# Kernel optimization log

Hardware: AMD Instinct MI355X
Metric: run time of the kernel (lower is better)

## Reference

```python
import jax, jax.numpy as jnp
import numpy as np

INPUT_SIZE, HIDDEN_SIZE, MEMORY_SIZE, SEQ_LEN, THETA = 512, 1024, 256, 4096, 4096.0
BATCH = 8


def _expm(M):
    # scaling-and-squaring Taylor expm (float64), replaces scipy cont2discrete's expm
    nrm = np.linalg.norm(M, 1)
    s = max(0, int(np.ceil(np.log2(max(nrm, 1.0)))) + 4)
    A = M / (2.0 ** s)
    E = np.eye(M.shape[0])
    T = np.eye(M.shape[0])
    for k in range(1, 24):
        T = T @ A / k
        E = E + T
    for _ in range(s):
        E = E @ E
    return E


def _lmu_H():
    # continuous-time Legendre state-space matrices
    Q = np.arange(MEMORY_SIZE, dtype=np.float64).reshape(-1, 1)
    R = (2.0 * Q + 1.0) / THETA
    i, j = np.meshgrid(Q.ravel(), Q.ravel(), indexing="ij")
    A = R * np.where(i < j, -1.0, (-1.0) ** (i - j + 1))
    B = R * (-1.0) ** Q
    # zero-order-hold discretization with dt=1: expm([[A,B],[0,0]])
    aug = np.zeros((MEMORY_SIZE + 1, MEMORY_SIZE + 1))
    aug[:MEMORY_SIZE, :MEMORY_SIZE] = A
    aug[:MEMORY_SIZE, MEMORY_SIZE:] = B
    Md = _expm(aug)
    Ad = Md[:MEMORY_SIZE, :MEMORY_SIZE].astype(np.float32)
    Bd = Md[:MEMORY_SIZE, MEMORY_SIZE:].astype(np.float32)
    # impulse response: H[:, t] = Ad^t @ Bd  (matches torch impulse() in float32)
    H = np.empty((MEMORY_SIZE, SEQ_LEN), dtype=np.float32)
    h = Bd[:, 0]
    for t in range(SEQ_LEN):
        H[:, t] = h
        h = Ad @ h
    return H


def setup_inputs():
    key = jax.random.key(0)
    k1, k2, k3, k4, k5 = jax.random.split(key, 5)
    x = jax.random.normal(k1, (BATCH, SEQ_LEN, INPUT_SIZE), jnp.float32)
    W_u_w = jax.random.normal(k2, (1, INPUT_SIZE), jnp.float32) / np.float32(np.sqrt(INPUT_SIZE))
    W_u_b = jax.random.normal(k3, (1,), jnp.float32) * 0.01
    W_h_w = jax.random.normal(k4, (HIDDEN_SIZE, MEMORY_SIZE + INPUT_SIZE), jnp.float32) / np.float32(np.sqrt(MEMORY_SIZE + INPUT_SIZE))
    W_h_b = jax.random.normal(k5, (HIDDEN_SIZE,), jnp.float32) * 0.01
    H = jnp.asarray(_lmu_H())
    return {"x": x, "W_u_w": W_u_w, "W_u_b": W_u_b, "W_h_w": W_h_w, "W_h_b": W_h_b, "H": H}


def reference(x, W_u_w, W_u_b, W_h_w, W_h_b, H):
    B, S, D = x.shape
    # u_t = relu(W_u x_t)  -> [B, S, 1]
    u = jax.nn.relu(jnp.einsum("bsd,od->bso", x, W_u_w) + W_u_b)
    # FFT long convolution of u with impulse response H (linear conv via 2S padding)
    fft_u = jnp.fft.rfft(u.transpose(0, 2, 1), n=2 * S, axis=-1)  # [B, 1, S+1]
    fft_H = jnp.fft.rfft(H, n=2 * S, axis=-1)                     # [M, S+1]
    m = jnp.fft.irfft(fft_u * fft_H[None], n=2 * S, axis=-1)[:, :, :S]  # [B, M, S]
    m = m.transpose(0, 2, 1)                                      # [B, S, M]
    # h_t = relu(W_h [m_t; x_t])
    h = jax.nn.relu(jnp.einsum("bsk,hk->bsh", jnp.concatenate([m, x], axis=-1), W_h_w) + W_h_b)
    return h, h[:, -1, :]
```

## Files before the change

kernel.cpp:

```cpp
#include <hip/hip_runtime.h>

typedef _Float16 half8 __attribute__((ext_vector_type(8)));
typedef float f32x4 __attribute__((ext_vector_type(4)));

#define SEQ   4096
#define DIN   512
#define HID   1024
#define KMEM  256
#define NB    8
#define KC    768
#define VP    4352
#define OUT_H_ELEMS 33554432ull

__device__ __forceinline__ void load_lds16(const void* g, void* l) {
  __builtin_amdgcn_global_load_lds(
      (const __attribute__((address_space(1))) unsigned int*)g,
      (__attribute__((address_space(3))) unsigned int*)l, 16, 0, 0);
}

__global__ __launch_bounds__(256) void u_kernel(
    const float* __restrict__ x, const float* __restrict__ Wu,
    const float* __restrict__ Wub,
    const float* __restrict__ Hf, const float* __restrict__ Wf,
    _Float16* __restrict__ xh, _Float16* __restrict__ v2,
    _Float16* __restrict__ Hh, _Float16* __restrict__ Wh)
{
  int tid_g = blockIdx.x * 256 + threadIdx.x;
  if (tid_g < KMEM * SEQ) Hh[tid_g] = (_Float16)Hf[tid_g];
  if (tid_g < HID * KC)   Wh[tid_g] = (_Float16)Wf[tid_g];
  if (tid_g < NB * 8 * 256) {
    int b2 = tid_g >> 11, rem = tid_g & 2047, p = rem >> 8, z = rem & 255;
    int t = (z < p) ? z : 4096 + z;
    v2[((size_t)b2 * 8 + p) * VP + t] = (_Float16)0.f;
  }

  int w = threadIdx.x >> 6, lane = threadIdx.x & 63;
  int row = blockIdx.x * 4 + w;
  const float4* xr = (const float4*)(x + (size_t)row * DIN);
  const float4* wr = (const float4*)Wu;
  float4 a0 = xr[lane * 2], a1 = xr[lane * 2 + 1];
  float4 w0 = wr[lane * 2], w1 = wr[lane * 2 + 1];
  float dot = a0.x * w0.x + a0.y * w0.y + a0.z * w0.z + a0.w * w0.w
            + a1.x * w1.x + a1.y * w1.y + a1.z * w1.z + a1.w * w1.w;
  half8 hv;
  hv[0] = (_Float16)a0.x; hv[1] = (_Float16)a0.y;
  hv[2] = (_Float16)a0.z; hv[3] = (_Float16)a0.w;
  hv[4] = (_Float16)a1.x; hv[5] = (_Float16)a1.y;
  hv[6] = (_Float16)a1.z; hv[7] = (_Float16)a1.w;
  *((half8*)(xh + (size_t)row * DIN + lane * 8)) = hv;
  #pragma unroll
  for (int off = 32; off > 0; off >>= 1) dot += __shfl_xor(dot, off);
  float u = dot + Wub[0];
  u = u > 0.f ? u : 0.f;
  if (lane < 8) {
    int s = row & (SEQ - 1), b = row >> 12;
    v2[(size_t)b * 8 * VP + (size_t)lane * VP + (4095 - s + lane)] = (_Float16)u;
  }
}

__global__ __launch_bounds__(256, 3) void conv_kernel(
    const _Float16* __restrict__ Hh, const _Float16* __restrict__ v2,
    _Float16* __restrict__ mh)
{
  __shared__ _Float16 Bs[2][128 * 64];
  __shared__ _Float16 Aw[2][8 * 208];
  int g = blockIdx.x;
  int cb = g & 15;
  int b = cb >> 1, kt = cb & 1;
  int jj = g >> 4;
  int its = (jj < 16) ? jj : (47 - jj);
  int s0 = its * 128, k0 = kt * 128;
  int tid = threadIdx.x;
  int w = tid >> 6, lane = tid & 63;
  int wr = w >> 1, wc = w & 1;
  int lm = lane & 15, q = lane >> 4;
  const _Float16* v2b = v2 + (size_t)b * 8 * VP;
  int gb = 3968 - s0;

  int aoffs[4];
  #pragma unroll
  for (int mi = 0; mi < 4; mi++) {
    int X = wr * 64 + mi * 16 + lm;
    int p = (X + 1) & 7;
    aoffs[mi] = p * 208 + (127 - X + p) + q * 8;
  }
  int boffs[4];
  #pragma unroll
  for (int ni = 0; ni < 4; ni++) {
    int col = wc * 64 + ni * 16 + lm;
    boffs[ni] = col * 64 + ((q ^ (lm & 7)) << 3);
  }

  int ap = tid / 26, aidx = tid - ap * 26;

  f32x4 acc[4][4] = {};
  int iters = 2 * (its + 1);

  {
    if (tid < 208)
      load_lds16(v2b + (size_t)ap * VP + gb + aidx * 8, Aw[0] + tid * 8);
    #pragma unroll
    for (int p2 = 0; p2 < 4; p2++) {
      int c = p2 * 256 + tid;
      int col = c >> 3, sl = c & 7;
      load_lds16(Hh + (size_t)(k0 + col) * SEQ + ((sl ^ (col & 7)) << 3),
                 Bs[0] + (size_t)c * 8);
    }
  }

  for (int it = 0; it < iters; ++it) {
    int buf = it & 1;
    __syncthreads();
    if (it + 1 < iters) {
      int r0 = (it + 1) * 64;
      if (tid < 208)
        load_lds16(v2b + (size_t)ap * VP + gb + r0 + aidx * 8, Aw[buf ^ 1] + tid * 8);
      #pragma unroll
      for (int p2 = 0; p2 < 4; p2++) {
        int c = p2 * 256 + tid;
        int col = c >> 3, sl = c & 7;
        load_lds16(Hh + (size_t)(k0 + col) * SEQ + r0 + ((sl ^ (col & 7)) << 3),
                   Bs[buf ^ 1] + (size_t)c * 8);
      }
    }
    #pragma unroll
    for (int kq = 0; kq < 2; kq++) {
      half8 af[4], bf[4];
      #pragma unroll
      for (int mi = 0; mi < 4; mi++)
        af[mi] = *((const half8*)(Aw[buf] + aoffs[mi] + kq * 32));
      #pragma unroll
      for (int ni = 0; ni < 4; ni++)
        bf[ni] = *((const half8*)(Bs[buf] + (boffs[ni] ^ (kq << 5))));
      #pragma unroll
      for (int mi = 0; mi < 4; mi++)
        #pragma unroll
        for (int ni = 0; ni < 4; ni++)
          acc[mi][ni] = __builtin_amdgcn_mfma_f32_16x16x32_f16(af[mi], bf[ni], acc[mi][ni], 0, 0, 0);
    }
  }
  size_t rowbase = (size_t)b * SEQ;
  #pragma unroll
  for (int mi = 0; mi < 4; mi++) {
    #pragma unroll
    for (int ni = 0; ni < 4; ni++) {
      int kout = k0 + wc * 64 + ni * 16 + lm;
      #pragma unroll
      for (int r = 0; r < 4; r++) {
        int sout = s0 + wr * 64 + mi * 16 + q * 4 + r;
        mh[(rowbase + sout) * KMEM + kout] = (_Float16)acc[mi][ni][r];
      }
    }
  }
}

__global__ __launch_bounds__(512, 4) void h_kernel(
    const _Float16* __restrict__ mh, const _Float16* __restrict__ xh,
    const _Float16* __restrict__ Wh, const float* __restrict__ Whb,
    float* __restrict__ out)
{
  __shared__ _Float16 As[2][128 * 32];
  __shared__ _Float16 Bs[2][256 * 32];
  int id = blockIdx.x;
  int wgid = (id & 7) * 128 + (id >> 3);
  int mt = wgid >> 2;
  int nt = wgid & 3;
  int tid = threadIdx.x, w = tid >> 6, lane = tid & 63;
  int wr = w >> 2, wc = w & 3;
  int lm = lane & 15, q = lane >> 4;

  int offM, offX;
  {
    int rowA = tid >> 2, chA = tid & 3;
    int swA = chA ^ ((rowA >> 2) & 3);
    offM = (mt * 128 + rowA) * KMEM + swA * 8;
    offX = (mt * 128 + rowA) * DIN  + swA * 8;
  }
  int offB[2];
  #pragma unroll
  for (int r = 0; r < 2; ++r) {
    int c = r * 512 + tid;
    int rowB = c >> 2, chB = c & 3;
    int swB = chB ^ ((rowB >> 2) & 3);
    offB[r] = (nt * 256 + rowB) * KC + swB * 8;
  }

  int qs = (q ^ ((lm >> 2) & 3)) << 3;
  int aoff[4], boff[4];
  #pragma unroll
  for (int mi = 0; mi < 4; ++mi) aoff[mi] = (wr * 64 + mi * 16 + lm) * 32 + qs;
  #pragma unroll
  for (int ni = 0; ni < 4; ++ni) boff[ni] = (wc * 64 + ni * 16 + lm) * 32 + qs;

  f32x4 acc[4][4] = {};
  {
    load_lds16(mh + offM, As[0] + tid * 8);
    #pragma unroll
    for (int r = 0; r < 2; ++r)
      load_lds16(Wh + offB[r], Bs[0] + (size_t)(r * 512 + tid) * 8);
  }

  for (int it = 0; it < 24; ++it) {
    int buf = it & 1;
    __syncthreads();
    if (it + 1 < 24) {
      int kk = (it + 1) * 32;
      const _Float16* srcA = (kk < KMEM) ? (mh + offM + kk)
                                         : (xh + offX + (kk - KMEM));
      load_lds16(srcA, As[buf ^ 1] + tid * 8);
      #pragma unroll
      for (int r = 0; r < 2; ++r)
        load_lds16(Wh + offB[r] + kk, Bs[buf ^ 1] + (size_t)(r * 512 + tid) * 8);
    }
    half8 af[4], bf[4];
    #pragma unroll
    for (int mi = 0; mi < 4; ++mi) af[mi] = *((const half8*)(As[buf] + aoff[mi]));
    #pragma unroll
    for (int ni = 0; ni < 4; ++ni) bf[ni] = *((const half8*)(Bs[buf] + boff[ni]));
    __builtin_amdgcn_s_setprio(1);
    #pragma unroll
    for (int mi = 0; mi < 4; ++mi)
      #pragma unroll
      for (int ni = 0; ni < 4; ++ni)
        acc[mi][ni] = __builtin_amdgcn_mfma_f32_16x16x32_f16(af[mi], bf[ni], acc[mi][ni], 0, 0, 0);
    __builtin_amdgcn_s_setprio(0);
  }

  #pragma unroll
  for (int ni = 0; ni < 4; ni++) {
    int colg = nt * 256 + wc * 64 + ni * 16 + lm;
    float bias = Whb[colg];
    #pragma unroll
    for (int mi = 0; mi < 4; mi++) {
      #pragma unroll
      for (int r = 0; r < 4; r++) {
        int rowg = mt * 128 + wr * 64 + mi * 16 + q * 4 + r;
        float v = acc[mi][ni][r] + bias;
        v = v > 0.f ? v : 0.f;
        __builtin_nontemporal_store(v, &out[(size_t)rowg * HID + colg]);
        if ((rowg & (SEQ - 1)) == SEQ - 1)
          __builtin_nontemporal_store(
              v, &out[OUT_H_ELEMS + (size_t)(rowg >> 12) * HID + colg]);
      }
    }
  }
}

extern "C" void kernel_launch(void* const* d_in, const int* in_sizes, int n_in,
                              void* d_out, int out_size, void* d_ws, size_t ws_size,
                              hipStream_t stream) {
  const float* x   = (const float*)d_in[0];
  const float* Wu  = (const float*)d_in[1];
  const float* Wub = (const float*)d_in[2];
  const float* Whw = (const float*)d_in[3];
  const float* Whb = (const float*)d_in[4];
  const float* Hf  = (const float*)d_in[5];
  float* out = (float*)d_out;

  char* ws = (char*)d_ws;
  _Float16* Hh = (_Float16*)(ws);
  _Float16* Wh = (_Float16*)(ws + 2097152);
  _Float16* v2 = (_Float16*)(ws + 3670016);
  _Float16* xh = (_Float16*)(ws + 4227072);
  _Float16* mh = (_Float16*)(ws + 37781504);

  u_kernel<<<dim3(8192), dim3(256), 0, stream>>>(x, Wu, Wub, Hf, Whw, xh, v2, Hh, Wh);
  conv_kernel<<<dim3(512), dim3(256), 0, stream>>>(Hh, v2, mh);
  h_kernel<<<dim3(1024), dim3(512), 0, stream>>>(mh, xh, Wh, Whb, out);
}
```

Baseline: 305.8 us.

## Load weight fragments directly from global memory and double K-step per stage

The h_kernel GEMM no longer stages the weight (B) tile in LDS. Each wave reads its B fragments straight from global memory into registers. The A tile is staged with a K-step of 64 instead of 32 and a new 8-way XOR swizzle, which halves the loop iterations and barriers. This removes the B-tile LDS traffic and frees LDS for occupancy, but it relies on L1/L2 hits for redundant weight reads across waves and exposes global load latency inside the loop.

```diff
diff --git a/kernel.cpp b/kernel.cpp
--- a/kernel.cpp
+++ b/kernel.cpp
@@ -159,8 +159,8 @@
     const _Float16* __restrict__ Wh, const float* __restrict__ Whb,
     float* __restrict__ out)
 {
-  __shared__ _Float16 As[2][128 * 32];
-  __shared__ _Float16 Bs[2][256 * 32];
+  __shared__ _Float16 As[2][128 * 64];
+
   int id = blockIdx.x;
   int wgid = (id & 7) * 128 + (id >> 3);
   int mt = wgid >> 2;
@@ -169,60 +169,67 @@
   int wr = w >> 2, wc = w & 3;
   int lm = lane & 15, q = lane >> 4;
 
-  int offM, offX;
-  {
-    int rowA = tid >> 2, chA = tid & 3;
-    int swA = chA ^ ((rowA >> 2) & 3);
-    offM = (mt * 128 + rowA) * KMEM + swA * 8;
-    offX = (mt * 128 + rowA) * DIN  + swA * 8;
-  }
-  int offB[2];
+  int offM[2], offX[2], ldsc[2];
   #pragma unroll
   for (int r = 0; r < 2; ++r) {
     int c = r * 512 + tid;
-    int rowB = c >> 2, chB = c & 3;
-    int swB = chB ^ ((rowB >> 2) & 3);
-    offB[r] = (nt * 256 + rowB) * KC + swB * 8;
-  }
-
-  int qs = (q ^ ((lm >> 2) & 3)) << 3;
-  int aoff[4], boff[4];
-  #pragma unroll
-  for (int mi = 0; mi < 4; ++mi) aoff[mi] = (wr * 64 + mi * 16 + lm) * 32 + qs;
-  #pragma unroll
-  for (int ni = 0; ni < 4; ++ni) boff[ni] = (wc * 64 + ni * 16 + lm) * 32 + qs;
+    int rowA = c >> 3, sl = c & 7;
+    int sw = sl ^ (rowA & 7);
+    offM[r] = (mt * 128 + rowA) * KMEM + sw * 8;
+    offX[r] = (mt * 128 + rowA) * DIN  + sw * 8;
+    ldsc[r] = c * 8;
+  }
+  int aoff[4];
+  #pragma unroll
+  for (int mi = 0; mi < 4; ++mi)
+    aoff[mi] = (wr * 64 + mi * 16 + lm) * 64 + ((q ^ (lm & 7)) << 3);
+
+  const _Float16* Bb = Wh + (size_t)(nt * 256 + wc * 64 + lm) * KC + q * 8;
 
   f32x4 acc[4][4] = {};
-  {
-    load_lds16(mh + offM, As[0] + tid * 8);
-    #pragma unroll
-    for (int r = 0; r < 2; ++r)
-      load_lds16(Wh + offB[r], Bs[0] + (size_t)(r * 512 + tid) * 8);
-  }
-
-  for (int it = 0; it < 24; ++it) {
+  #pragma unroll
+  for (int r = 0; r < 2; ++r)
+    load_lds16(mh + offM[r], As[0] + ldsc[r]);
+
+  for (int it = 0; it < 12; ++it) {
     int buf = it & 1;
+    int kk = it * 64;
     __syncthreads();
-    if (it + 1 < 24) {
-      int kk = (it + 1) * 32;
-      const _Float16* srcA = (kk < KMEM) ? (mh + offM + kk)
-                                         : (xh + offX + (kk - KMEM));
-      load_lds16(srcA, As[buf ^ 1] + tid * 8);
-      #pragma unroll
-      for (int r = 0; r < 2; ++r)
-        load_lds16(Wh + offB[r] + kk, Bs[buf ^ 1] + (size_t)(r * 512 + tid) * 8);
-    }
-    half8 af[4], bf[4];
-    #pragma unroll
-    for (int mi = 0; mi < 4; ++mi) af[mi] = *((const half8*)(As[buf] + aoff[mi]));
-    #pragma unroll
-    for (int ni = 0; ni < 4; ++ni) bf[ni] = *((const half8*)(Bs[buf] + boff[ni]));
+    half8 bf0[4], bf1[4];
+    #pragma unroll
+    for (int ni = 0; ni < 4; ++ni)
+      bf0[ni] = *((const half8*)(Bb + (size_t)(ni * 16) * KC + kk));
+    #pragma unroll
+    for (int ni = 0; ni < 4; ++ni)
+      bf1[ni] = *((const half8*)(Bb + (size_t)(ni * 16) * KC + kk + 32));
+    if (it + 1 < 12) {
+      int kn = (it + 1) * 64;
+      #pragma unroll
+      for (int r = 0; r < 2; ++r) {
+        const _Float16* sa = (kn < KMEM) ? (mh + offM[r] + kn)
+                                         : (xh + offX[r] + (kn - KMEM));
+        load_lds16(sa, As[buf ^ 1] + ldsc[r]);
+      }
+    }
+    const _Float16* la = As[buf];
+    half8 af[4];
+    #pragma unroll
+    for (int mi = 0; mi < 4; ++mi) af[mi] = *((const half8*)(la + aoff[mi]));
     __builtin_amdgcn_s_setprio(1);
     #pragma unroll
     for (int mi = 0; mi < 4; ++mi)
       #pragma unroll
       for (int ni = 0; ni < 4; ++ni)
-        acc[mi][ni] = __builtin_amdgcn_mfma_f32_16x16x32_f16(af[mi], bf[ni], acc[mi][ni], 0, 0, 0);
+        acc[mi][ni] = __builtin_amdgcn_mfma_f32_16x16x32_f16(af[mi], bf0[ni], acc[mi][ni], 0, 0, 0);
+    __builtin_amdgcn_s_setprio(0);
+    #pragma unroll
+    for (int mi = 0; mi < 4; ++mi) af[mi] = *((const half8*)(la + (aoff[mi] ^ 32)));
+    __builtin_amdgcn_s_setprio(1);
+    #pragma unroll
+    for (int mi = 0; mi < 4; ++mi)
+      #pragma unroll
+      for (int ni = 0; ni < 4; ++ni)
+        acc[mi][ni] = __builtin_amdgcn_mfma_f32_16x16x32_f16(af[mi], bf1[ni], acc[mi][ni], 0, 0, 0);
     __builtin_amdgcn_s_setprio(0);
   }
 
```

Result: slower. 350.5 us (+14.6%).
